# Kernel tuning notes

Hardware: AMD Instinct MI355X
Metric: run time of the kernel (lower is better)

Reference implementation:

```python
import jax, jax.numpy as jnp
import numpy as np

N, E, IN, H, K = 50000, 800000, 64, 128, 16
EPS = 1e-15


def setup_inputs() -> dict:
    key = jax.random.key(0)
    ks = jax.random.split(key, 8)
    x = jax.random.normal(ks[0], (N, IN), jnp.float32)
    edge_index = jax.random.randint(ks[1], (2, E), 0, N)
    edge_weight = jax.random.uniform(ks[2], (E,), jnp.float32)
    # GCNConv(normalize=False) params: lin weight (no lin bias) + additive bias
    W1 = jax.random.normal(ks[3], (IN, H), jnp.float32) / np.sqrt(IN)
    b1 = jnp.zeros((H,), jnp.float32)
    W2 = jax.random.normal(ks[4], (H, H), jnp.float32) / np.sqrt(H)
    b2 = jnp.zeros((H,), jnp.float32)
    # MLP head: single Linear(H, K) since mlp_units=[]
    Wm = jax.random.normal(ks[5], (H, K), jnp.float32) / np.sqrt(H)
    bm = jnp.zeros((K,), jnp.float32)
    return {"x": x, "edge_index": edge_index, "edge_weight": edge_weight,
            "W1": W1, "b1": b1, "W2": W2, "b2": b2, "Wm": Wm, "bm": bm}


def _gcn(h_in, W, b, src, dst, w):
    # GCNConv with normalize=False, cached=False: no self-loops, no degree norm.
    # out_i = sum_{(j->i) in E} w_ji * (x_j @ W) + b
    h = h_in @ W                         # [N, out] dense transform first
    msg = h[src] * w[:, None]            # [E, out] gather + edge scale
    agg = jax.ops.segment_sum(msg, dst, num_segments=N)  # scatter-add
    return agg + b


def reference(x, edge_index, edge_weight, W1, b1, W2, b2, Wm, bm):
    src, dst = edge_index[0], edge_index[1]
    h = jax.nn.relu(_gcn(x, W1, b1, src, dst, edge_weight))
    h = jax.nn.relu(_gcn(h, W2, b2, src, dst, edge_weight))
    s = h @ Wm + bm                      # cluster logits [N, K]
    sm = jax.nn.softmax(s, axis=-1)      # soft assignments S
    # just_balance_pool balance loss: -trace(sqrt(S^T S + EPS)) elementwise-sqrt,
    # i.e. -sum_k sqrt(sum_i S_ik^2 + EPS), normalized by sqrt(N*K).
    diag = jnp.sum(sm * sm, axis=0)      # [K] = diag(S^T S)
    loss = -jnp.sum(jnp.sqrt(diag + EPS))
    loss = loss / jnp.sqrt(jnp.asarray(N * K, sm.dtype))
    return sm, loss
```

## Files before the change

### kernel.cpp

```cpp
#include <hip/hip_runtime.h>
#include <hip/hip_fp16.h>
#include <math.h>

static constexpr int N_NODES = 50000;
static constexpr int E_EDGES = 800000;
static constexpr int IN_F = 64;
static constexpr int H_F = 128;
static constexpr int K_C = 16;
static constexpr int BUCK_SHIFT = 7;
static constexpr int NBUCK = (N_NODES + 127) >> BUCK_SHIFT;
static constexpr int CHUNK_E = 4096;
static constexpr int NCHUNK = (E_EDGES + CHUNK_E - 1) / CHUNK_E;
static constexpr int BUCK_CAP = 4096;
static constexpr int PREP_B = 3221;

typedef _Float16 h4 __attribute__((ext_vector_type(4)));
typedef _Float16 h8 __attribute__((ext_vector_type(8)));
typedef float f4 __attribute__((ext_vector_type(4)));

__device__ __forceinline__ void unpack(unsigned int e, int& s, float& w) {
  s = (int)(e & 0xffffu);
  w = __half2float(__ushort_as_half((unsigned short)(e >> 16)));
}

__global__ __launch_bounds__(256) void prep_hist(
    const float* __restrict__ x, __half* __restrict__ xh,
    const float* __restrict__ W1, __half* __restrict__ WT1,
    const float* __restrict__ W2, __half* __restrict__ WT2,
    const int* __restrict__ dst, int* __restrict__ bcount) {
  __shared__ int lh[NBUCK];
  if (blockIdx.x < PREP_B) {
    const int i = blockIdx.x * 256 + threadIdx.x;
    const int n4 = N_NODES * IN_F / 4;
    if (i < n4) {
      float4 v = ((const float4*)x)[i];
      __half2* o = (__half2*)xh + (size_t)i * 2;
      o[0] = __floats2half2_rn(v.x, v.y);
      o[1] = __floats2half2_rn(v.z, v.w);
    }
    const int j = i - n4;
    if (j >= 0 && j < IN_F * 128) {
      const int k = j >> 7, col = j & 127;
      unsigned boff = (unsigned)((col * IN_F + k) * 2) ^ (unsigned)((col & 7) << 4);
      *(__half*)((char*)WT1 + boff) = __float2half_rn(W1[j]);
    }
    const int k2 = j - IN_F * 128;
    if (k2 >= 0 && k2 < H_F * 128) {
      const int k = k2 >> 7, col = k2 & 127;
      unsigned boff = (unsigned)((col * H_F + k) * 2) ^ (unsigned)((col & 7) << 4);
      *(__half*)((char*)WT2 + boff) = __float2half_rn(W2[k2]);
    }
  } else {
    const int cb = blockIdx.x - PREP_B;
    for (int i = threadIdx.x; i < NBUCK; i += 256) lh[i] = 0;
    __syncthreads();
    const int e0 = cb * CHUNK_E;
    const int cnt = min(CHUNK_E, E_EDGES - e0);
    for (int i = threadIdx.x; i < cnt; i += 256)
      atomicAdd(&lh[dst[e0 + i] >> BUCK_SHIFT], 1);
    __syncthreads();
    for (int i = threadIdx.x; i < NBUCK; i += 256)
      if (lh[i]) atomicAdd(&bcount[i], lh[i]);
  }
}

__global__ __launch_bounds__(64) void bscan_kernel(
    const int* __restrict__ bcount, int* __restrict__ bbase, int* __restrict__ bcursor) {
  const int t = threadIdx.x;
  int carry = 0;
  for (int base = 0; base < NBUCK; base += 64) {
    const int idx = base + t;
    const int v = (idx < NBUCK) ? bcount[idx] : 0;
    int inc = v;
#pragma unroll
    for (int d = 1; d < 64; d <<= 1) {
      int u = __shfl_up(inc, d);
      if (t >= d) inc += u;
    }
    if (idx < NBUCK) {
      const int ex = carry + inc - v;
      bbase[idx] = ex;
      bcursor[idx] = ex;
    }
    carry += __shfl(inc, 63);
  }
  if (t == 0) bbase[NBUCK] = E_EDGES;
}

__global__ __launch_bounds__(256) void bin_pass(
    const int* __restrict__ src, const int* __restrict__ dst,
    const float* __restrict__ w, int* __restrict__ bcursor,
    int2* __restrict__ inter) {
  __shared__ int lhist[NBUCK];
  __shared__ int lstart[NBUCK];
  __shared__ int bbase_s[NBUCK];
  __shared__ int2 stage[CHUNK_E];
  const int e0 = blockIdx.x * CHUNK_E;
  const int cnt = min(CHUNK_E, E_EDGES - e0);

  for (int i = threadIdx.x; i < NBUCK; i += 256) lhist[i] = 0;
  __syncthreads();
  for (int i = threadIdx.x; i < cnt; i += 256)
    atomicAdd(&lhist[dst[e0 + i] >> BUCK_SHIFT], 1);
  __syncthreads();

  if (threadIdx.x < 64) {
    const int lane = threadIdx.x;
    int carry = 0;
    for (int base = 0; base < NBUCK; base += 64) {
      const int idx = base + lane;
      const int v = (idx < NBUCK) ? lhist[idx] : 0;
      int inc = v;
#pragma unroll
      for (int d = 1; d < 64; d <<= 1) {
        int u = __shfl_up(inc, d);
        if (lane >= d) inc += u;
      }
      if (idx < NBUCK) lstart[idx] = carry + inc - v;
      carry += __shfl(inc, 63);
    }
  }
  __syncthreads();

  for (int b = threadIdx.x; b < NBUCK; b += 256) {
    const int c = lhist[b];
    bbase_s[b] = (c > 0) ? atomicAdd(&bcursor[b], c) : 0;
    lhist[b] = lstart[b];
  }
  __syncthreads();

  for (int i = threadIdx.x; i < cnt; i += 256) {
    const int d = dst[e0 + i];
    const int b = d >> BUCK_SHIFT;
    const int pos = atomicAdd(&lhist[b], 1);
    const unsigned short wb = __half_as_ushort(__float2half_rn(w[e0 + i]));
    stage[pos] = make_int2(src[e0 + i] | ((d & 127) << 16),
                           (int)wb | (b << 16));
  }
  __syncthreads();

  for (int i = threadIdx.x; i < cnt; i += 256) {
    const int2 en = stage[i];
    const int b = (en.y >> 16) & 0x1ff;
    inter[bbase_s[b] + (i - lstart[b])] = en;
  }
}

__global__ __launch_bounds__(256) void sortoff_pass(
    const int2* __restrict__ inter, const int* __restrict__ bbase,
    unsigned int* __restrict__ csr, int* __restrict__ off) {
  __shared__ int lhist[128];
  __shared__ int lstart[128];
  __shared__ unsigned int outbuf[BUCK_CAP];
  const int b = blockIdx.x;
  const int n0 = b << BUCK_SHIFT;
  const int r0 = bbase[b];
  const int r1 = bbase[b + 1];
  const int cnt = r1 - r0;

  if (threadIdx.x < 128) lhist[threadIdx.x] = 0;
  __syncthreads();
  for (int i = threadIdx.x; i < cnt; i += 256)
    atomicAdd(&lhist[(inter[r0 + i].x >> 16) & 127], 1);
  __syncthreads();

  if (threadIdx.x < 64) {
    const int lane = threadIdx.x;
    int carry = 0;
#pragma unroll
    for (int base = 0; base < 128; base += 64) {
      const int v = lhist[base + lane];
      int inc = v;
#pragma unroll
      for (int d = 1; d < 64; d <<= 1) {
        int u = __shfl_up(inc, d);
        if (lane >= d) inc += u;
      }
      lstart[base + lane] = carry + inc - v;
      carry += __shfl(inc, 63);
    }
  }
  __syncthreads();

  if (threadIdx.x < 128) {
    const int nn = n0 + threadIdx.x;
    if (nn < N_NODES) off[nn] = r0 + lstart[threadIdx.x];
    lhist[threadIdx.x] = lstart[threadIdx.x];
  }
  if (b == NBUCK - 1 && threadIdx.x == 0) off[N_NODES] = E_EDGES;
  __syncthreads();

  for (int i = threadIdx.x; i < cnt; i += 256) {
    const int2 en = inter[r0 + i];
    const int dlo = (en.x >> 16) & 127;
    const int pos = atomicAdd(&lhist[dlo], 1);
    outbuf[pos] = (unsigned int)(en.x & 0xffff) |
                  ((unsigned int)(en.y & 0xffff) << 16);
  }
  __syncthreads();
  for (int i = threadIdx.x; i < cnt; i += 256) csr[r0 + i] = outbuf[i];
}

__global__ __launch_bounds__(256) void gather_x(
    const __half* __restrict__ t, const int* __restrict__ off,
    const unsigned int* __restrict__ csr, __half* __restrict__ outb) {
  const int node = blockIdx.x * 4 + (threadIdx.x >> 6);
  const int l = threadIdx.x & 63;
  const int g = l >> 4;
  const int f0 = (l & 15) * 4;
  const int p0 = off[node], p1 = off[node + 1];
  f4 a0 = {0.f, 0.f, 0.f, 0.f}, a1 = {0.f, 0.f, 0.f, 0.f};
  int p = p0;
  for (; p + 16 <= p1; p += 16) {
    int s[4]; float w[4]; h4 v[4];
#pragma unroll
    for (int u = 0; u < 4; ++u) unpack(csr[p + 4 * u + g], s[u], w[u]);
#pragma unroll
    for (int u = 0; u < 4; ++u) v[u] = *(const h4*)(t + (size_t)s[u] * IN_F + f0);
#pragma unroll
    for (int u = 0; u < 4; ++u) {
      f4& a = (u & 1) ? a1 : a0;
      a.x = fmaf((float)v[u].x, w[u], a.x); a.y = fmaf((float)v[u].y, w[u], a.y);
      a.z = fmaf((float)v[u].z, w[u], a.z); a.w = fmaf((float)v[u].w, w[u], a.w);
    }
  }
  if (p < p1) {
    int s[4]; float w[4]; h4 v[4];
#pragma unroll
    for (int u = 0; u < 4; ++u) {
      const int idx = p + 4 * u + g;
      unpack(csr[min(idx, p1 - 1)], s[u], w[u]);
      if (idx >= p1) w[u] = 0.f;
    }
#pragma unroll
    for (int u = 0; u < 4; ++u) v[u] = *(const h4*)(t + (size_t)s[u] * IN_F + f0);
#pragma unroll
    for (int u = 0; u < 4; ++u) {
      f4& a = (u & 1) ? a1 : a0;
      a.x = fmaf((float)v[u].x, w[u], a.x); a.y = fmaf((float)v[u].y, w[u], a.y);
      a.z = fmaf((float)v[u].z, w[u], a.z); a.w = fmaf((float)v[u].w, w[u], a.w);
    }
  }
  a0.x += a1.x; a0.y += a1.y; a0.z += a1.z; a0.w += a1.w;
  a0.x += __shfl_xor(a0.x, 16); a0.y += __shfl_xor(a0.y, 16);
  a0.z += __shfl_xor(a0.z, 16); a0.w += __shfl_xor(a0.w, 16);
  a0.x += __shfl_xor(a0.x, 32); a0.y += __shfl_xor(a0.y, 32);
  a0.z += __shfl_xor(a0.z, 32); a0.w += __shfl_xor(a0.w, 32);
  if (l < 16) {
    h4 o;
    o.x = (_Float16)a0.x; o.y = (_Float16)a0.y;
    o.z = (_Float16)a0.z; o.w = (_Float16)a0.w;
    *(h4*)(outb + (size_t)node * IN_F + f0) = o;
  }
}

template<int K, bool BIAS_RELU>
__global__ __launch_bounds__(256) void gemm_mfma(
    const __half* __restrict__ A, const __half* __restrict__ WT,
    const float* __restrict__ bias, __half* __restrict__ out, int n) {
  __shared__ _Float16 Wl[128 * K];
  for (int t = threadIdx.x; t < 128 * K / 8; t += 256)
    ((uint4*)Wl)[t] = ((const uint4*)WT)[t];
  __syncthreads();

  const int wv = threadIdx.x >> 6;
  const int l = threadIdx.x & 63;
  const int row = l & 15, kg = l >> 4;
  const int r0 = blockIdx.x * 64 + wv * 16;
  const int ar = min(r0 + row, n - 1);

  h8 af[K / 32];
#pragma unroll
  for (int ks = 0; ks < K / 32; ++ks)
    af[ks] = *(const h8*)(A + (size_t)ar * K + ks * 32 + kg * 8);

  const unsigned swz = (unsigned)((row & 7) << 4);
#pragma unroll
  for (int c = 0; c < 8; ++c) {
    const int col = c * 16 + row;
    f4 acc = {0.f, 0.f, 0.f, 0.f};
#pragma unroll
    for (int ks = 0; ks < K / 32; ++ks) {
      const unsigned boff = ((unsigned)((col * K + ks * 32 + kg * 8) * 2)) ^ swz;
      const h8 bf = *(const h8*)((const char*)Wl + boff);
      acc = __builtin_amdgcn_mfma_f32_16x16x32_f16(af[ks], bf, acc, 0, 0, 0);
    }
    const float bb = BIAS_RELU ? bias[col] : 0.f;
#pragma unroll
    for (int q = 0; q < 4; ++q) {
      const int rr = r0 + kg * 4 + q;
      if (rr < n) {
        float v = acc[q];
        if (BIAS_RELU) v = fmaxf(v + bb, 0.f);
        out[(size_t)rr * H_F + col] = __float2half_rn(v);
      }
    }
  }
}

__global__ __launch_bounds__(256) void gather_h(
    const __half* __restrict__ t, const int* __restrict__ off,
    const unsigned int* __restrict__ csr, __half* __restrict__ outb) {
  const int node = blockIdx.x * 4 + (threadIdx.x >> 6);
  const int lane = threadIdx.x & 63;
  const __half2* __restrict__ tb = (const __half2*)t;
  const int p0 = off[node], p1 = off[node + 1];
  float2 a[4];
#pragma unroll
  for (int i = 0; i < 4; ++i) a[i] = make_float2(0.f, 0.f);
  int p = p0;
  for (; p + 16 <= p1; p += 16) {
    int s[16]; float w[16]; __half2 hv[16];
#pragma unroll
    for (int i = 0; i < 16; ++i) unpack(csr[p + i], s[i], w[i]);
#pragma unroll
    for (int i = 0; i < 16; ++i) hv[i] = tb[(size_t)s[i] * 64 + lane];
#pragma unroll
    for (int i = 0; i < 16; ++i) {
      const float2 f = __half22float2(hv[i]);
      a[i & 3].x = fmaf(f.x, w[i], a[i & 3].x);
      a[i & 3].y = fmaf(f.y, w[i], a[i & 3].y);
    }
  }
  if (p < p1) {
    int s[16]; float w[16]; __half2 hv[16];
#pragma unroll
    for (int i = 0; i < 16; ++i) {
      unpack(csr[min(p + i, p1 - 1)], s[i], w[i]);
      if (p + i >= p1) w[i] = 0.f;
    }
#pragma unroll
    for (int i = 0; i < 16; ++i) hv[i] = tb[(size_t)s[i] * 64 + lane];
#pragma unroll
    for (int i = 0; i < 16; ++i) {
      const float2 f = __half22float2(hv[i]);
      a[i & 3].x = fmaf(f.x, w[i], a[i & 3].x);
      a[i & 3].y = fmaf(f.y, w[i], a[i & 3].y);
    }
  }
  const float2 s2 = make_float2((a[0].x + a[1].x) + (a[2].x + a[3].x),
                                (a[0].y + a[1].y) + (a[2].y + a[3].y));
  ((__half2*)outb)[(size_t)node * 64 + lane] = __float22half2_rn(s2);
}

__global__ __launch_bounds__(256) void head_kernel(
    const __half* __restrict__ h2raw, const float* __restrict__ b2,
    const float* __restrict__ Wm, const float* __restrict__ bm,
    float* __restrict__ sm_out, float* __restrict__ diag, int n) {
  __shared__ float Wl[H_F * K_C];
  __shared__ float b2l[H_F];
  __shared__ float part[K_C];
  for (int t = threadIdx.x; t < H_F * K_C; t += 256) Wl[t] = Wm[t];
  if (threadIdx.x < H_F) b2l[threadIdx.x] = b2[threadIdx.x];
  if (threadIdx.x < K_C) part[threadIdx.x] = 0.f;
  __syncthreads();

  const int node = blockIdx.x * 256 + threadIdx.x;
  const int lane = threadIdx.x & 63;
  float acc[K_C];
#pragma unroll
  for (int c = 0; c < K_C; ++c) acc[c] = bm[c];

  if (node < n) {
    const __half2* __restrict__ hrow = (const __half2*)(h2raw + (size_t)node * H_F);
#pragma unroll 4
    for (int k2 = 0; k2 < H_F / 2; ++k2) {
      const float2 hv = __half22float2(hrow[k2]);
      const float h0 = fmaxf(hv.x + b2l[2 * k2], 0.f);
      const float h1 = fmaxf(hv.y + b2l[2 * k2 + 1], 0.f);
      const float4* __restrict__ w0 = (const float4*)(Wl + (2 * k2) * K_C);
      const float4* __restrict__ w1 = (const float4*)(Wl + (2 * k2 + 1) * K_C);
#pragma unroll
      for (int q = 0; q < 4; ++q) {
        const float4 aa = w0[q], bb = w1[q];
        acc[4 * q + 0] = fmaf(h0, aa.x, acc[4 * q + 0]);
        acc[4 * q + 1] = fmaf(h0, aa.y, acc[4 * q + 1]);
        acc[4 * q + 2] = fmaf(h0, aa.z, acc[4 * q + 2]);
        acc[4 * q + 3] = fmaf(h0, aa.w, acc[4 * q + 3]);
        acc[4 * q + 0] = fmaf(h1, bb.x, acc[4 * q + 0]);
        acc[4 * q + 1] = fmaf(h1, bb.y, acc[4 * q + 1]);
        acc[4 * q + 2] = fmaf(h1, bb.z, acc[4 * q + 2]);
        acc[4 * q + 3] = fmaf(h1, bb.w, acc[4 * q + 3]);
      }
    }
  }

  float mx = acc[0];
#pragma unroll
  for (int c = 1; c < K_C; ++c) mx = fmaxf(mx, acc[c]);
  float sum = 0.f;
#pragma unroll
  for (int c = 0; c < K_C; ++c) { acc[c] = __expf(acc[c] - mx); sum += acc[c]; }
  const float inv = 1.f / sum;
  float sq[K_C];
  if (node < n) {
#pragma unroll
    for (int c = 0; c < K_C; ++c) { acc[c] *= inv; sq[c] = acc[c] * acc[c]; }
    float4* o = (float4*)(sm_out + (size_t)node * K_C);
    o[0] = make_float4(acc[0], acc[1], acc[2], acc[3]);
    o[1] = make_float4(acc[4], acc[5], acc[6], acc[7]);
    o[2] = make_float4(acc[8], acc[9], acc[10], acc[11]);
    o[3] = make_float4(acc[12], acc[13], acc[14], acc[15]);
  } else {
#pragma unroll
    for (int c = 0; c < K_C; ++c) sq[c] = 0.f;
  }

#pragma unroll
  for (int c = 0; c < K_C; ++c) {
    float v = sq[c];
#pragma unroll
    for (int off2 = 32; off2; off2 >>= 1) v += __shfl_xor(v, off2);
    if (lane == 0) atomicAdd(&part[c], v);
  }
  __syncthreads();
  if (threadIdx.x < K_C) atomicAdd(&diag[threadIdx.x], part[threadIdx.x]);
}

__global__ void loss_kernel(const float* __restrict__ diag, float* __restrict__ out) {
  int c = threadIdx.x;
  float v = (c < K_C) ? sqrtf(diag[c] + 1e-15f) : 0.f;
#pragma unroll
  for (int off2 = 8; off2; off2 >>= 1) v += __shfl_xor(v, off2, 16);
  if (c == 0) out[0] = -v / sqrtf((float)N_NODES * (float)K_C);
}

extern "C" void kernel_launch(void* const* d_in, const int* in_sizes, int n_in,
                              void* d_out, int out_size, void* d_ws, size_t ws_size,
                              hipStream_t stream) {
  const float* x  = (const float*)d_in[0];
  const int*   ei = (const int*)d_in[1];
  const float* ew = (const float*)d_in[2];
  const float* W1 = (const float*)d_in[3];
  const float* b1 = (const float*)d_in[4];
  const float* W2 = (const float*)d_in[5];
  const float* b2 = (const float*)d_in[6];
  const float* Wm = (const float*)d_in[7];
  const float* bm = (const float*)d_in[8];
  float* out = (float*)d_out;

  const int* srcv = ei;
  const int* dstv = ei + E_EDGES;

  char* ws = (char*)d_ws;
  float*        diag    = (float*)ws;
  int*          bcount  = (int*)(ws + 64);
  int*          bbase   = (int*)(ws + 2048);
  int*          bcursor = (int*)(ws + 4096);
  __half*       WT1     = (__half*)(ws + 8192);
  __half*       WT2     = (__half*)(ws + 8192 + 16384);
  int*          off     = (int*)(ws + 65536);
  unsigned int* csr     = (unsigned int*)(off + N_NODES + 64);
  int2*         inter   = (int2*)(csr + E_EDGES);
  char*         bufA    = (char*)(inter + E_EDGES);
  char*         bufB    = bufA + (size_t)N_NODES * H_F * 2;

  __half* xh    = (__half*)bufB;
  __half* aggxh = (__half*)bufA;
  __half* h1h   = (__half*)bufB;
  __half* t2h   = (__half*)bufA;
  __half* h2h   = (__half*)bufB;

  hipMemsetAsync(ws, 0, 2048, stream);

  prep_hist<<<PREP_B + NCHUNK, 256, 0, stream>>>(x, xh, W1, WT1, W2, WT2, dstv, bcount);

  bscan_kernel<<<1, 64, 0, stream>>>(bcount, bbase, bcursor);
  bin_pass<<<NCHUNK, 256, 0, stream>>>(srcv, dstv, ew, bcursor, inter);
  sortoff_pass<<<NBUCK, 256, 0, stream>>>(inter, bbase, csr, off);

  gather_x<<<N_NODES / 4, 256, 0, stream>>>(xh, off, csr, aggxh);
  gemm_mfma<IN_F, true><<<(N_NODES + 63) / 64, 256, 0, stream>>>(aggxh, WT1, b1, h1h, N_NODES);

  gemm_mfma<H_F, false><<<(N_NODES + 63) / 64, 256, 0, stream>>>(h1h, WT2, nullptr, t2h, N_NODES);
  gather_h<<<N_NODES / 4, 256, 0, stream>>>(t2h, off, csr, h2h);

  head_kernel<<<(N_NODES + 255) / 256, 256, 0, stream>>>(h2h, b2, Wm, bm, out, diag, N_NODES);
  loss_kernel<<<1, 64, 0, stream>>>(diag, out + (size_t)N_NODES * K_C);
}
```

Measured before the change: 150.2 us.

## Fold bucket scan into bin pass, loss into head, two nodes per wave in gather_h

Drops the single-block bucket-scan kernel by having every bin_pass block redundantly compute the global exclusive scan of bucket counts. It also folds the loss computation into head_kernel using a last-block atomic counter, removing two kernel launches. gather_h now processes two consecutive nodes per wavefront so their tail loads can be issued together. The costs are duplicated scan work in each bin_pass block, higher register pressure in gather_h, and a fence plus atomic at the end of head_kernel.

```diff
diff --git a/kernel.cpp b/kernel.cpp
--- a/kernel.cpp
+++ b/kernel.cpp
@@ -64,32 +64,10 @@
   }
 }
 
-__global__ __launch_bounds__(64) void bscan_kernel(
-    const int* __restrict__ bcount, int* __restrict__ bbase, int* __restrict__ bcursor) {
-  const int t = threadIdx.x;
-  int carry = 0;
-  for (int base = 0; base < NBUCK; base += 64) {
-    const int idx = base + t;
-    const int v = (idx < NBUCK) ? bcount[idx] : 0;
-    int inc = v;
-#pragma unroll
-    for (int d = 1; d < 64; d <<= 1) {
-      int u = __shfl_up(inc, d);
-      if (t >= d) inc += u;
-    }
-    if (idx < NBUCK) {
-      const int ex = carry + inc - v;
-      bbase[idx] = ex;
-      bcursor[idx] = ex;
-    }
-    carry += __shfl(inc, 63);
-  }
-  if (t == 0) bbase[NBUCK] = E_EDGES;
-}
-
 __global__ __launch_bounds__(256) void bin_pass(
     const int* __restrict__ src, const int* __restrict__ dst,
-    const float* __restrict__ w, int* __restrict__ bcursor,
+    const float* __restrict__ w, const int* __restrict__ bcount,
+    int* __restrict__ bcursor, int* __restrict__ bbase_g,
     int2* __restrict__ inter) {
   __shared__ int lhist[NBUCK];
   __shared__ int lstart[NBUCK];
@@ -106,25 +84,34 @@
 
   if (threadIdx.x < 64) {
     const int lane = threadIdx.x;
-    int carry = 0;
+    int carry = 0, carryG = 0;
     for (int base = 0; base < NBUCK; base += 64) {
       const int idx = base + lane;
-      const int v = (idx < NBUCK) ? lhist[idx] : 0;
-      int inc = v;
+      const int v  = (idx < NBUCK) ? lhist[idx] : 0;
+      const int vg = (idx < NBUCK) ? bcount[idx] : 0;
+      int inc = v, incG = vg;
 #pragma unroll
       for (int d = 1; d < 64; d <<= 1) {
-        int u = __shfl_up(inc, d);
-        if (lane >= d) inc += u;
+        int u  = __shfl_up(inc, d);
+        int uG = __shfl_up(incG, d);
+        if (lane >= d) { inc += u; incG += uG; }
       }
-      if (idx < NBUCK) lstart[idx] = carry + inc - v;
-      carry += __shfl(inc, 63);
-    }
+      if (idx < NBUCK) {
+        lstart[idx] = carry + inc - v;
+        const int gb = carryG + incG - vg;
+        bbase_s[idx] = gb;
+        bbase_g[idx] = gb;
+      }
+      carry  += __shfl(inc, 63);
+      carryG += __shfl(incG, 63);
+    }
+    if (lane == 0) bbase_g[NBUCK] = E_EDGES;
   }
   __syncthreads();
 
   for (int b = threadIdx.x; b < NBUCK; b += 256) {
     const int c = lhist[b];
-    bbase_s[b] = (c > 0) ? atomicAdd(&bcursor[b], c) : 0;
+    bbase_s[b] += (c > 0) ? atomicAdd(&bcursor[b], c) : 0;
     lhist[b] = lstart[b];
   }
   __syncthreads();
@@ -301,15 +288,18 @@
 __global__ __launch_bounds__(256) void gather_h(
     const __half* __restrict__ t, const int* __restrict__ off,
     const unsigned int* __restrict__ csr, __half* __restrict__ outb) {
-  const int node = blockIdx.x * 4 + (threadIdx.x >> 6);
+  const int nodeA = blockIdx.x * 8 + ((threadIdx.x >> 6) * 2);
   const int lane = threadIdx.x & 63;
   const __half2* __restrict__ tb = (const __half2*)t;
-  const int p0 = off[node], p1 = off[node + 1];
-  float2 a[4];
-#pragma unroll
-  for (int i = 0; i < 4; ++i) a[i] = make_float2(0.f, 0.f);
-  int p = p0;
-  for (; p + 16 <= p1; p += 16) {
+  const int pa0 = off[nodeA];
+  const int pm  = off[nodeA + 1];
+  const int pb1 = off[nodeA + 2];
+
+  float2 aA0 = {0.f, 0.f}, aA1 = {0.f, 0.f};
+  float2 aB0 = {0.f, 0.f}, aB1 = {0.f, 0.f};
+
+  int p = pa0;
+  for (; pm - p > 16; p += 16) {
     int s[16]; float w[16]; __half2 hv[16];
 #pragma unroll
     for (int i = 0; i < 16; ++i) unpack(csr[p + i], s[i], w[i]);
@@ -318,38 +308,80 @@
 #pragma unroll
     for (int i = 0; i < 16; ++i) {
       const float2 f = __half22float2(hv[i]);
-      a[i & 3].x = fmaf(f.x, w[i], a[i & 3].x);
-      a[i & 3].y = fmaf(f.y, w[i], a[i & 3].y);
-    }
-  }
-  if (p < p1) {
+      float2& a = (i & 1) ? aA1 : aA0;
+      a.x = fmaf(f.x, w[i], a.x); a.y = fmaf(f.y, w[i], a.y);
+    }
+  }
+  int q = pm;
+  for (; pb1 - q > 16; q += 16) {
     int s[16]; float w[16]; __half2 hv[16];
 #pragma unroll
-    for (int i = 0; i < 16; ++i) {
-      unpack(csr[min(p + i, p1 - 1)], s[i], w[i]);
-      if (p + i >= p1) w[i] = 0.f;
-    }
+    for (int i = 0; i < 16; ++i) unpack(csr[q + i], s[i], w[i]);
 #pragma unroll
     for (int i = 0; i < 16; ++i) hv[i] = tb[(size_t)s[i] * 64 + lane];
 #pragma unroll
     for (int i = 0; i < 16; ++i) {
       const float2 f = __half22float2(hv[i]);
-      a[i & 3].x = fmaf(f.x, w[i], a[i & 3].x);
-      a[i & 3].y = fmaf(f.y, w[i], a[i & 3].y);
-    }
-  }
-  const float2 s2 = make_float2((a[0].x + a[1].x) + (a[2].x + a[3].x),
-                                (a[0].y + a[1].y) + (a[2].y + a[3].y));
-  ((__half2*)outb)[(size_t)node * 64 + lane] = __float22half2_rn(s2);
+      float2& a = (i & 1) ? aB1 : aB0;
+      a.x = fmaf(f.x, w[i], a.x); a.y = fmaf(f.y, w[i], a.y);
+    }
+  }
+
+  const bool anyA = p < pm, anyB = q < pb1;
+  int sA[16]; float wA[16]; __half2 hA[16];
+  int sB[16]; float wB[16]; __half2 hB[16];
+  if (anyA) {
+#pragma unroll
+    for (int i = 0; i < 16; ++i) {
+      const int idx = p + i;
+      unpack(csr[min(idx, pm - 1)], sA[i], wA[i]);
+      if (idx >= pm) wA[i] = 0.f;
+    }
+#pragma unroll
+    for (int i = 0; i < 16; ++i) hA[i] = tb[(size_t)sA[i] * 64 + lane];
+  }
+  if (anyB) {
+#pragma unroll
+    for (int i = 0; i < 16; ++i) {
+      const int idx = q + i;
+      unpack(csr[min(idx, pb1 - 1)], sB[i], wB[i]);
+      if (idx >= pb1) wB[i] = 0.f;
+    }
+#pragma unroll
+    for (int i = 0; i < 16; ++i) hB[i] = tb[(size_t)sB[i] * 64 + lane];
+  }
+  if (anyA) {
+#pragma unroll
+    for (int i = 0; i < 16; ++i) {
+      const float2 f = __half22float2(hA[i]);
+      float2& a = (i & 1) ? aA1 : aA0;
+      a.x = fmaf(f.x, wA[i], a.x); a.y = fmaf(f.y, wA[i], a.y);
+    }
+  }
+  if (anyB) {
+#pragma unroll
+    for (int i = 0; i < 16; ++i) {
+      const float2 f = __half22float2(hB[i]);
+      float2& a = (i & 1) ? aB1 : aB0;
+      a.x = fmaf(f.x, wB[i], a.x); a.y = fmaf(f.y, wB[i], a.y);
+    }
+  }
+
+  const float2 rA = make_float2(aA0.x + aA1.x, aA0.y + aA1.y);
+  const float2 rB = make_float2(aB0.x + aB1.x, aB0.y + aB1.y);
+  ((__half2*)outb)[(size_t)nodeA * 64 + lane]       = __float22half2_rn(rA);
+  ((__half2*)outb)[(size_t)(nodeA + 1) * 64 + lane] = __float22half2_rn(rB);
 }
 
 __global__ __launch_bounds__(256) void head_kernel(
     const __half* __restrict__ h2raw, const float* __restrict__ b2,
     const float* __restrict__ Wm, const float* __restrict__ bm,
-    float* __restrict__ sm_out, float* __restrict__ diag, int n) {
+    float* __restrict__ sm_out, float* __restrict__ diag,
+    unsigned int* __restrict__ ctr, float* __restrict__ loss_out, int n) {
   __shared__ float Wl[H_F * K_C];
   __shared__ float b2l[H_F];
   __shared__ float part[K_C];
+  __shared__ int lastf;
   for (int t = threadIdx.x; t < H_F * K_C; t += 256) Wl[t] = Wm[t];
   if (threadIdx.x < H_F) b2l[threadIdx.x] = b2[threadIdx.x];
   if (threadIdx.x < K_C) part[threadIdx.x] = 0.f;
@@ -371,16 +403,16 @@
       const float4* __restrict__ w0 = (const float4*)(Wl + (2 * k2) * K_C);
       const float4* __restrict__ w1 = (const float4*)(Wl + (2 * k2 + 1) * K_C);
 #pragma unroll
-      for (int q = 0; q < 4; ++q) {
-        const float4 aa = w0[q], bb = w1[q];
-        acc[4 * q + 0] = fmaf(h0, aa.x, acc[4 * q + 0]);
-        acc[4 * q + 1] = fmaf(h0, aa.y, acc[4 * q + 1]);
-        acc[4 * q + 2] = fmaf(h0, aa.z, acc[4 * q + 2]);
-        acc[4 * q + 3] = fmaf(h0, aa.w, acc[4 * q + 3]);
-        acc[4 * q + 0] = fmaf(h1, bb.x, acc[4 * q + 0]);
-        acc[4 * q + 1] = fmaf(h1, bb.y, acc[4 * q + 1]);
-        acc[4 * q + 2] = fmaf(h1, bb.z, acc[4 * q + 2]);
-        acc[4 * q + 3] = fmaf(h1, bb.w, acc[4 * q + 3]);
+      for (int qq = 0; qq < 4; ++qq) {
+        const float4 aa = w0[qq], bb = w1[qq];
+        acc[4 * qq + 0] = fmaf(h0, aa.x, acc[4 * qq + 0]);
+        acc[4 * qq + 1] = fmaf(h0, aa.y, acc[4 * qq + 1]);
+        acc[4 * qq + 2] = fmaf(h0, aa.z, acc[4 * qq + 2]);
+        acc[4 * qq + 3] = fmaf(h0, aa.w, acc[4 * qq + 3]);
+        acc[4 * qq + 0] = fmaf(h1, bb.x, acc[4 * qq + 0]);
+        acc[4 * qq + 1] = fmaf(h1, bb.y, acc[4 * qq + 1]);
+        acc[4 * qq + 2] = fmaf(h1, bb.z, acc[4 * qq + 2]);
+        acc[4 * qq + 3] = fmaf(h1, bb.w, acc[4 * qq + 3]);
       }
     }
   }
@@ -415,14 +447,19 @@
   }
   __syncthreads();
   if (threadIdx.x < K_C) atomicAdd(&diag[threadIdx.x], part[threadIdx.x]);
-}
-
-__global__ void loss_kernel(const float* __restrict__ diag, float* __restrict__ out) {
-  int c = threadIdx.x;
-  float v = (c < K_C) ? sqrtf(diag[c] + 1e-15f) : 0.f;
-#pragma unroll
-  for (int off2 = 8; off2; off2 >>= 1) v += __shfl_xor(v, off2, 16);
-  if (c == 0) out[0] = -v / sqrtf((float)N_NODES * (float)K_C);
+  __syncthreads();
+  __threadfence();
+  if (threadIdx.x == 0)
+    lastf = (atomicAdd(ctr, 1u) == (unsigned)(gridDim.x - 1)) ? 1 : 0;
+  __syncthreads();
+  if (lastf && threadIdx.x < 64) {
+    const int c = threadIdx.x;
+    float v = 0.f;
+    if (c < K_C) v = sqrtf(atomicAdd(&diag[c], 0.f) + 1e-15f);
+#pragma unroll
+    for (int off2 = 8; off2; off2 >>= 1) v += __shfl_xor(v, off2, 16);
+    if (c == 0) loss_out[0] = -v / sqrtf((float)N_NODES * (float)K_C);
+  }
 }
 
 extern "C" void kernel_launch(void* const* d_in, const int* in_sizes, int n_in,
@@ -444,9 +481,10 @@
 
   char* ws = (char*)d_ws;
   float*        diag    = (float*)ws;
-  int*          bcount  = (int*)(ws + 64);
-  int*          bbase   = (int*)(ws + 2048);
-  int*          bcursor = (int*)(ws + 4096);
+  unsigned int* ctr     = (unsigned int*)(ws + 64);
+  int*          bcount  = (int*)(ws + 128);
+  int*          bcursor = (int*)(ws + 2048);
+  int*          bbase   = (int*)(ws + 4096);
   __half*       WT1     = (__half*)(ws + 8192);
   __half*       WT2     = (__half*)(ws + 8192 + 16384);
   int*          off     = (int*)(ws + 65536);
@@ -461,20 +499,19 @@
   __half* t2h   = (__half*)bufA;
   __half* h2h   = (__half*)bufB;
 
-  hipMemsetAsync(ws, 0, 2048, stream);
+  hipMemsetAsync(ws, 0, 4096, stream);
 
   prep_hist<<<PREP_B + NCHUNK, 256, 0, stream>>>(x, xh, W1, WT1, W2, WT2, dstv, bcount);
 
-  bscan_kernel<<<1, 64, 0, stream>>>(bcount, bbase, bcursor);
-  bin_pass<<<NCHUNK, 256, 0, stream>>>(srcv, dstv, ew, bcursor, inter);
+  bin_pass<<<NCHUNK, 256, 0, stream>>>(srcv, dstv, ew, bcount, bcursor, bbase, inter);
   sortoff_pass<<<NBUCK, 256, 0, stream>>>(inter, bbase, csr, off);
 
   gather_x<<<N_NODES / 4, 256, 0, stream>>>(xh, off, csr, aggxh);
   gemm_mfma<IN_F, true><<<(N_NODES + 63) / 64, 256, 0, stream>>>(aggxh, WT1, b1, h1h, N_NODES);
 
   gemm_mfma<H_F, false><<<(N_NODES + 63) / 64, 256, 0, stream>>>(h1h, WT2, nullptr, t2h, N_NODES);
-  gather_h<<<N_NODES / 4, 256, 0, stream>>>(t2h, off, csr, h2h);
-
-  head_kernel<<<(N_NODES + 255) / 256, 256, 0, stream>>>(h2h, b2, Wm, bm, out, diag, N_NODES);
-  loss_kernel<<<1, 64, 0, stream>>>(diag, out + (size_t)N_NODES * K_C);
-}
+  gather_h<<<N_NODES / 8, 256, 0, stream>>>(t2h, off, csr, h2h);
+
+  head_kernel<<<(N_NODES + 255) / 256, 256, 0, stream>>>(
+      h2h, b2, Wm, bm, out, diag, ctr, out + (size_t)N_NODES * K_C, N_NODES);
+}
```

After: 156.5 us. 4.2% more time.
